# Kernel optimization log

Measured on AMD Instinct MI355X. Metric: run time of the kernel, lower is better.

Reference implementation:

```python
import jax, jax.numpy as jnp
import numpy as np

# Dims: batch, seq, model dim, heads, routes-per-query, bleed-over alpha
B, S, D, H, K_ROUTES = 4, 512, 1024, 16, 64
HD = D // H                      # head_dim = 64
SCALE = 1.0 / float(np.sqrt(HD))
ALPHA = 0.25                     # neighbor bleed-over (forward arg default 0.0; >0 here)
CAUSAL = True
NEG = jnp.float32(-1e9)


def _build_routes(seq_len: int, k: int, depth: int = 8) -> np.ndarray:
    """Cantor-coordinate based positional routes (mirrors _build_positional_routes)."""
    pos = np.arange(seq_len, dtype=np.float64)
    x = pos / max(1, seq_len - 1)
    x = np.clip(x, 1e-6, 1.0 - 1e-6)
    val = np.zeros_like(x)
    factor = 0.5
    for _ in range(depth):
        xs = x * 3.0
        digit = xs.astype(np.int64)
        frac = xs - digit
        val = val + (digit == 2).astype(np.float64) * factor
        x = frac
        factor *= 0.5
    coords = np.clip(val, 0.0, 1.0)
    dist = np.abs(coords[:, None] - coords[None, :])            # [S,S]
    routes = np.argsort(dist, axis=1, kind='stable')[:, :k]     # k smallest distances
    return routes.astype(np.int32)


def setup_inputs() -> dict:
    key = jax.random.key(0)
    k0, k1, k2 = jax.random.split(key, 3)
    x = jax.random.normal(k0, (B, S, D), dtype=jnp.float32)
    # nn.Linear weights stored pre-transposed as [in, out] for clean matmul
    w_qkv = jax.random.normal(k1, (D, 3 * D), dtype=jnp.float32) * (1.0 / np.sqrt(D))
    b_qkv = jnp.zeros((3 * D,), dtype=jnp.float32)
    w_out = jax.random.normal(k2, (D, D), dtype=jnp.float32) * (1.0 / np.sqrt(D))
    b_out = jnp.zeros((D,), dtype=jnp.float32)
    routes = jnp.asarray(_build_routes(S, K_ROUTES), dtype=jnp.int32)  # [S, K]
    return {"x": x, "w_qkv": w_qkv, "b_qkv": b_qkv,
            "w_out": w_out, "b_out": b_out, "routes": routes}


def reference(x, w_qkv, b_qkv, w_out, b_out, routes):
    # QKV projection: [B,S,3D] -> [3,B,H,S,hd]
    qkv = (x @ w_qkv + b_qkv).reshape(B, S, 3, H, HD).transpose(2, 0, 3, 1, 4)
    q, k, v = qkv[0], qkv[1], qkv[2]                 # each [B,H,S,hd]

    r = routes                                        # [S,K]
    k_g = jnp.take(k, r, axis=2)                      # [B,H,S,K,hd]
    v_g = jnp.take(v, r, axis=2)
    if ALPHA > 0.0:
        rl = jnp.clip(r - 1, 0, S - 1)
        rr = jnp.clip(r + 1, 0, S - 1)
        k_g = (1.0 - ALPHA) * k_g + (ALPHA / 2.0) * (jnp.take(k, rl, axis=2) + jnp.take(k, rr, axis=2))
        v_g = (1.0 - ALPHA) * v_g + (ALPHA / 2.0) * (jnp.take(v, rl, axis=2) + jnp.take(v, rr, axis=2))

    scores = jnp.einsum('bhqd,bhqkd->bhqk', q, k_g) * SCALE   # [B,H,S,K]
    if CAUSAL:
        # route index > query position is masked (each query always routes to itself)
        mask = r > jnp.arange(S, dtype=r.dtype)[:, None]       # [S,K]
        scores = jnp.where(mask[None, None], NEG, scores)

    attn = jax.nn.softmax(scores, axis=-1)
    out = jnp.einsum('bhqk,bhqkd->bhqd', attn, v_g)            # [B,H,S,hd]
    out = out.transpose(0, 2, 1, 3).reshape(B, S, D)
    return out @ w_out + b_out
```

## Files before the change

### kernel.cpp

```cpp
#include <hip/hip_runtime.h>
#include <hip/hip_bf16.h>

#define BB 4
#define SS 512
#define DD 1024
#define HH 16
#define KR 64
#define HDIM 64
#define THREE_D 3072
#define M_ROWS 2048
#define SCALE_F 0.125f

typedef __attribute__((ext_vector_type(8))) short short8;
typedef __attribute__((ext_vector_type(4))) float floatx4;

union F8 { short8 s; unsigned int u[4]; unsigned short h[8]; };

__device__ inline float bfu(unsigned short h){ union{unsigned int u; float f;} c; c.u = ((unsigned int)h) << 16; return c.f; }
__device__ inline unsigned short f2bf(float f){
    union{float f; unsigned int u;} c; c.f = f;
    unsigned int u = c.u;
    return (unsigned short)((u + 0x7fffu + ((u >> 16) & 1u)) >> 16);
}

#define GLOAD_LDS16(g, l)                                                     \
    __builtin_amdgcn_global_load_lds(                                         \
        (const __attribute__((address_space(1))) unsigned int*)(g),           \
        (__attribute__((address_space(3))) unsigned int*)(l), 16, 0, 0)

__global__ __launch_bounds__(256) void cvtA_kernel(const float* __restrict__ x,
                                                   unsigned short* __restrict__ out)
{
    int gid = blockIdx.x * 256 + threadIdx.x;
    int r  = gid & 127;
    int c  = (gid >> 7) & 3;
    int kt = (gid >> 9) & 31;
    int mt = gid >> 14;
    const float* src = x + ((size_t)(mt * 128 + r)) * 1024 + kt * 32 + c * 8;
    float4 a = *(const float4*)src;
    float4 b = *(const float4*)(src + 4);
    F8 o;
    o.h[0] = f2bf(a.x); o.h[1] = f2bf(a.y); o.h[2] = f2bf(a.z); o.h[3] = f2bf(a.w);
    o.h[4] = f2bf(b.x); o.h[5] = f2bf(b.y); o.h[6] = f2bf(b.z); o.h[7] = f2bf(b.w);
    *(uint4*)(out + (size_t)gid * 8) = *(uint4*)&o;
}

__global__ __launch_bounds__(256) void cvtB_kernel(const float* __restrict__ w,
                                                   unsigned short* __restrict__ out, int N)
{
    int gid = blockIdx.x * 256 + threadIdx.x;
    int r  = gid & 127;
    int c  = (gid >> 7) & 3;
    int kt = (gid >> 9) & 31;
    int nt = gid >> 14;
    int n = nt * 128 + r;
    int kbase = kt * 32 + c * 8;
    F8 o;
#pragma unroll
    for (int j = 0; j < 8; ++j)
        o.h[j] = f2bf(w[(size_t)(kbase + j) * N + n]);
    *(uint4*)(out + (size_t)gid * 8) = *(uint4*)&o;
}

__global__ __launch_bounds__(256) void gemm_qkv(
    const unsigned short* __restrict__ Asw,
    const unsigned short* __restrict__ Bsw,
    const float* __restrict__ bias,
    unsigned short* __restrict__ qb, unsigned short* __restrict__ kb,
    unsigned short* __restrict__ vb)
{
    __shared__ __align__(16) unsigned short Sh[128 * 136];
    unsigned short* Alds = Sh;
    unsigned short* Blds = Sh + 4096;

    const int tid  = threadIdx.x;
    const int lane = tid & 63;
    const int wid  = tid >> 6;
    const int l15  = lane & 15;
    const int quad = lane >> 4;
    const int wm   = (wid >> 1) * 64;
    const int wn   = (wid & 1) * 64;

    const unsigned short* Ak = Asw + (size_t)blockIdx.y * 131072;
    const unsigned short* Bk = Bsw + (size_t)blockIdx.x * 131072;

    floatx4 acc[4][4];
#pragma unroll
    for (int i = 0; i < 4; ++i)
#pragma unroll
        for (int j = 0; j < 4; ++j) acc[i][j] = (floatx4){0.f, 0.f, 0.f, 0.f};

    for (int kt = 0; kt < 32; ++kt) {
        const unsigned short* ga = Ak + kt * 4096 + wid * 1024 + lane * 8;
        const unsigned short* gb = Bk + kt * 4096 + wid * 1024 + lane * 8;
        GLOAD_LDS16(ga,       Alds + wid * 1024);
        GLOAD_LDS16(ga + 512, Alds + wid * 1024 + 512);
        GLOAD_LDS16(gb,       Blds + wid * 1024);
        GLOAD_LDS16(gb + 512, Blds + wid * 1024 + 512);
        __syncthreads();

        F8 af[4], bf[4];
#pragma unroll
        for (int mi = 0; mi < 4; ++mi)
            af[mi] = *(const F8*)(Alds + (size_t)(quad * 128 + wm + mi * 16 + l15) * 8);
#pragma unroll
        for (int ni = 0; ni < 4; ++ni)
            bf[ni] = *(const F8*)(Blds + (size_t)(quad * 128 + wn + ni * 16 + l15) * 8);
#pragma unroll
        for (int mi = 0; mi < 4; ++mi)
#pragma unroll
            for (int ni = 0; ni < 4; ++ni)
                acc[mi][ni] = __builtin_amdgcn_mfma_f32_16x16x32_bf16(
                    af[mi].s, bf[ni].s, acc[mi][ni], 0, 0, 0);
        __syncthreads();
    }

    const int m0 = blockIdx.y * 128;
    const int n0 = blockIdx.x * 128;

#pragma unroll
    for (int mi = 0; mi < 4; ++mi) {
#pragma unroll
        for (int ni = 0; ni < 4; ++ni) {
            int col = wn + ni * 16 + l15;
            float bv = bias[n0 + col];
#pragma unroll
            for (int r = 0; r < 4; ++r) {
                int row = wm + mi * 16 + quad * 4 + r;
                Sh[row * 136 + col] = f2bf(acc[mi][ni][r] + bv);
            }
        }
    }
    __syncthreads();

    for (int i = tid; i < 2048; i += 256) {
        int rr = i >> 4, cc = i & 15;
        int grow = m0 + rr, gcol = n0 + cc * 8;
        int b = grow >> 9, s = grow & 511;
        int which = gcol >> 10, rem = gcol & 1023;
        int h = rem >> 6, hd = rem & 63;
        unsigned short* dst = (which == 0) ? qb : (which == 1) ? kb : vb;
        uint4 val = *(const uint4*)(Sh + rr * 136 + cc * 8);
        *(uint4*)(dst + (((size_t)(b * HH + h) * SS) + s) * HDIM + hd) = val;
    }
}

__global__ __launch_bounds__(256) void gemm_out(
    const unsigned short* __restrict__ Asw,
    const unsigned short* __restrict__ Bsw,
    const float* __restrict__ bias,
    float* __restrict__ Cout)
{
    __shared__ __align__(16) unsigned short Alds[2048];
    __shared__ __align__(16) unsigned short Blds[4096];

    const int tid  = threadIdx.x;
    const int lane = tid & 63;
    const int wid  = tid >> 6;
    const int l15  = lane & 15;
    const int quad = lane >> 4;
    const int mt64 = blockIdx.y;
    const int mt   = mt64 >> 1;
    const int rh   = (mt64 & 1) * 64;
    const int nt   = blockIdx.x;
    const int wn   = wid * 32;

    floatx4 acc[4][2];
#pragma unroll
    for (int i = 0; i < 4; ++i)
#pragma unroll
        for (int j = 0; j < 2; ++j) acc[i][j] = (floatx4){0.f, 0.f, 0.f, 0.f};

    for (int kt = 0; kt < 32; ++kt) {
        const unsigned short* ga = Asw + ((size_t)(mt * 32 + kt) * 4 + wid) * 1024 + (rh + lane) * 8;
        const unsigned short* gb = Bsw + (size_t)(nt * 32 + kt) * 4096 + wid * 1024 + lane * 8;
        GLOAD_LDS16(ga,       Alds + (wid * 64 + lane) * 8);
        GLOAD_LDS16(gb,       Blds + wid * 1024 + lane * 8);
        GLOAD_LDS16(gb + 512, Blds + wid * 1024 + 512 + lane * 8);
        __syncthreads();

        F8 af[4], bf[2];
#pragma unroll
        for (int mi = 0; mi < 4; ++mi)
            af[mi] = *(const F8*)(Alds + (size_t)(quad * 64 + mi * 16 + l15) * 8);
#pragma unroll
        for (int ni = 0; ni < 2; ++ni)
            bf[ni] = *(const F8*)(Blds + (size_t)(quad * 128 + wn + ni * 16 + l15) * 8);
#pragma unroll
        for (int mi = 0; mi < 4; ++mi)
#pragma unroll
            for (int ni = 0; ni < 2; ++ni)
                acc[mi][ni] = __builtin_amdgcn_mfma_f32_16x16x32_bf16(
                    af[mi].s, bf[ni].s, acc[mi][ni], 0, 0, 0);
        __syncthreads();
    }

    const int m0 = mt64 * 64;
    const int n0 = nt * 128;
#pragma unroll
    for (int mi = 0; mi < 4; ++mi) {
#pragma unroll
        for (int ni = 0; ni < 2; ++ni) {
            int col = n0 + wn + ni * 16 + l15;
            float bv = bias[col];
#pragma unroll
            for (int r = 0; r < 4; ++r) {
                int row = m0 + mi * 16 + quad * 4 + r;
                Cout[(size_t)row * DD + col] = acc[mi][ni][r] + bv;
            }
        }
    }
}

__global__ __launch_bounds__(256) void blend_tr_kernel(
    const unsigned short* __restrict__ kb, const unsigned short* __restrict__ vb,
    unsigned short* __restrict__ K2g, unsigned short* __restrict__ Vtg)
{
    __shared__ float kt[130][65];
    __shared__ float vt[130][65];
    const int bh = blockIdx.x >> 2;
    const int sb = (blockIdx.x & 3) * 128;
    const int tid = threadIdx.x;
    const unsigned short* kbase = kb + (size_t)bh * SS * HDIM;
    const unsigned short* vbase = vb + (size_t)bh * SS * HDIM;

    for (int i = tid; i < 130 * 8; i += 256) {
        int row = i >> 3, c8 = (i & 7) << 3;
        int s = sb + row - 1; s = s < 0 ? 0 : (s > SS - 1 ? SS - 1 : s);
        F8 kk = *(const F8*)(kbase + (size_t)s * 64 + c8);
        F8 vv = *(const F8*)(vbase + (size_t)s * 64 + c8);
#pragma unroll
        for (int j = 0; j < 8; ++j) {
            kt[row][c8 + j] = bfu(kk.h[j]);
            vt[row][c8 + j] = bfu(vv.h[j]);
        }
    }
    __syncthreads();

    for (int i = tid; i < 128 * 16; i += 256) {
        int sl = i >> 4, c4 = (i & 15) << 2;
        ushort4 o;
        o.x = f2bf(0.75f * kt[sl+1][c4+0] + 0.125f * (kt[sl][c4+0] + kt[sl+2][c4+0]));
        o.y = f2bf(0.75f * kt[sl+1][c4+1] + 0.125f * (kt[sl][c4+1] + kt[sl+2][c4+1]));
        o.z = f2bf(0.75f * kt[sl+1][c4+2] + 0.125f * (kt[sl][c4+2] + kt[sl+2][c4+2]));
        o.w = f2bf(0.75f * kt[sl+1][c4+3] + 0.125f * (kt[sl][c4+3] + kt[sl+2][c4+3]));
        *(ushort4*)(K2g + ((size_t)bh * SS + sb + sl) * 64 + c4) = o;
    }
    for (int i = tid; i < 64 * 32; i += 256) {
        int d = i >> 5, s4 = (i & 31) << 2;
        ushort4 o;
        o.x = f2bf(0.75f * vt[s4+1][d] + 0.125f * (vt[s4+0][d] + vt[s4+2][d]));
        o.y = f2bf(0.75f * vt[s4+2][d] + 0.125f * (vt[s4+1][d] + vt[s4+3][d]));
        o.z = f2bf(0.75f * vt[s4+3][d] + 0.125f * (vt[s4+2][d] + vt[s4+4][d]));
        o.w = f2bf(0.75f * vt[s4+4][d] + 0.125f * (vt[s4+3][d] + vt[s4+5][d]));
        *(ushort4*)(Vtg + ((size_t)bh * 64 + d) * SS + sb + s4) = o;
    }
}

__global__ __launch_bounds__(256) void mask_kernel(const int* __restrict__ routes,
                                                   unsigned int* __restrict__ maskg)
{
    int q = blockIdx.x * 256 + threadIdx.x;
    unsigned int w[16];
#pragma unroll
    for (int i = 0; i < 16; ++i) w[i] = 0u;
    for (int j = 0; j < KR; ++j) {
        int r = routes[q * KR + j];
        if (r <= q) w[r >> 5] |= 1u << (r & 31);
    }
#pragma unroll
    for (int sw = 0; sw < 16; ++sw) maskg[sw * SS + q] = w[sw];
}

__global__ __launch_bounds__(512, 2) void attn_kernel(
    const unsigned short* __restrict__ qb,
    const unsigned short* __restrict__ K2g,
    const unsigned short* __restrict__ Vtg,
    const unsigned int* __restrict__ maskg,
    unsigned short* __restrict__ attn_sw)
{
    __shared__ __align__(16) unsigned short Ks[512 * 64];
    __shared__ __align__(16) unsigned short Vs[64 * 512];
    __shared__ __align__(16) unsigned short Ps[8 * 16 * 64];

    const int bh = blockIdx.x >> 2;
    const int qt = blockIdx.x & 3;
    const int b = bh >> 4, h = bh & 15;
    const int tid  = threadIdx.x;
    const int lane = tid & 63;
    const int wid  = tid >> 6;
    const int l15  = lane & 15;
    const int quad = lane >> 4;

    {
        const uint4* src = (const uint4*)(K2g + (size_t)bh * (SS * 64));
        uint4* dst = (uint4*)Ks;
        for (int c = tid; c < 4096; c += 512) {
            int s = c >> 3, cc = c & 7;
            dst[(s << 3) | (cc ^ (s & 7))] = src[c];
        }
        const uint4* srcv = (const uint4*)(Vtg + (size_t)bh * (64 * SS));
        uint4* dstv = (uint4*)Vs;
        for (int c = tid; c < 4096; c += 512) {
            int d = c >> 6, sc = c & 63;
            dstv[(d << 6) | (sc & 56) | ((sc ^ d) & 7)] = srcv[c];
        }
    }
    __syncthreads();

    const int qbase = qt * 128 + wid * 16;
    const int q = qbase + l15;

    F8 qf[2];
    {
        const unsigned short* qrow = qb + ((size_t)bh * SS + q) * 64;
        qf[0] = *(const F8*)(qrow + quad * 8);
        qf[1] = *(const F8*)(qrow + 32 + quad * 8);
    }

    floatx4 accS[32];
#pragma unroll
    for (int st = 0; st < 32; ++st) {
        int srow = st * 16 + l15;
        const F8 k0 = *(const F8*)(Ks + (((srow << 3) | ( quad      ^ (srow & 7))) << 3));
        const F8 k1 = *(const F8*)(Ks + (((srow << 3) | ((4 + quad) ^ (srow & 7))) << 3));
        floatx4 a = (floatx4){0.f, 0.f, 0.f, 0.f};
        a = __builtin_amdgcn_mfma_f32_16x16x32_bf16(k0.s, qf[0].s, a, 0, 0, 0);
        a = __builtin_amdgcn_mfma_f32_16x16x32_bf16(k1.s, qf[1].s, a, 0, 0, 0);
        accS[st] = a;
    }

    float m = -1e30f;
    unsigned int mw = 0;
#pragma unroll
    for (int st = 0; st < 32; ++st) {
        if ((st & 1) == 0) mw = maskg[(st >> 1) * SS + q];
        int sbase = (st & 1) * 16 + quad * 4;
        floatx4 a = accS[st];
#pragma unroll
        for (int r = 0; r < 4; ++r) {
            float v = ((mw >> (sbase + r)) & 1u) ? a[r] * SCALE_F : -1e30f;
            a[r] = v;
            m = fmaxf(m, v);
        }
        accS[st] = a;
    }
    m = fmaxf(m, __shfl_xor(m, 16));
    m = fmaxf(m, __shfl_xor(m, 32));

    floatx4 accO[4];
#pragma unroll
    for (int dt = 0; dt < 4; ++dt) accO[dt] = (floatx4){0.f, 0.f, 0.f, 0.f};
    float lsum = 0.f;
    unsigned int* Pw = (unsigned int*)Ps + wid * 512;

#pragma unroll
    for (int ch = 0; ch < 8; ++ch) {
#pragma unroll
        for (int t = 0; t < 4; ++t) {
            floatx4 a = accS[ch * 4 + t];
            float e0 = __expf(a[0] - m), e1 = __expf(a[1] - m);
            float e2 = __expf(a[2] - m), e3 = __expf(a[3] - m);
            lsum += (e0 + e1) + (e2 + e3);
            unsigned int w0 = (unsigned int)f2bf(e0) | ((unsigned int)f2bf(e1) << 16);
            unsigned int w1 = (unsigned int)f2bf(e2) | ((unsigned int)f2bf(e3) << 16);
            int off0 = t * 8 + quad * 2;
            int off1 = off0 + 1;
            Pw[l15 * 32 + ((((off0 >> 2) ^ (l15 & 7)) << 2) | (off0 & 3))] = w0;
            Pw[l15 * 32 + ((((off1 >> 2) ^ (l15 & 7)) << 2) | (off1 & 3))] = w1;
        }
        F8 pa[2];
#pragma unroll
        for (int ks = 0; ks < 2; ++ks) {
            int ci = ks * 4 + quad;
            pa[ks] = *(const F8*)((const unsigned short*)(Pw + l15 * 32) +
                                  ((ci ^ (l15 & 7)) << 3));
        }
#pragma unroll
        for (int dt = 0; dt < 4; ++dt) {
            int d = dt * 16 + l15;
#pragma unroll
            for (int ks = 0; ks < 2; ++ks) {
                int sc = ch * 8 + ks * 4 + quad;
                const F8 bv = *(const F8*)(Vs + (((d << 6) | (sc & 56) | ((sc ^ d) & 7)) << 3));
                accO[dt] = __builtin_amdgcn_mfma_f32_16x16x32_bf16(pa[ks].s, bv.s, accO[dt], 0, 0, 0);
            }
        }
    }

    lsum += __shfl_xor(lsum, 16);
    lsum += __shfl_xor(lsum, 32);
    float inv = 1.0f / lsum;

    unsigned short* Ow = Ps + wid * 1024;
#pragma unroll
    for (int r = 0; r < 4; ++r) {
        float invr = __shfl(inv, quad * 4 + r);
#pragma unroll
        for (int dt = 0; dt < 4; ++dt)
            Ow[(quad * 4 + r) * 64 + dt * 16 + l15] = f2bf(accO[dt][r] * invr);
    }
#pragma unroll
    for (int i = 0; i < 2; ++i) {
        int ch = i * 64 + lane;
        int qlocal = ch >> 3, j = ch & 7;
        int qq = qt * 128 + wid * 16 + qlocal;
        int mrow = b * SS + qq;
        int mt = mrow >> 7, rr = mrow & 127;
        int kt2 = h * 2 + (j >> 2), c = j & 3;
        size_t gid = (((size_t)(mt * 32 + kt2) * 4 + c) * 128 + rr);
        *(uint4*)(attn_sw + gid * 8) = *(const uint4*)(Ow + qlocal * 64 + j * 8);
    }
}

extern "C" void kernel_launch(void* const* d_in, const int* in_sizes, int n_in,
                              void* d_out, int out_size, void* d_ws, size_t ws_size,
                              hipStream_t stream)
{
    const float* x     = (const float*)d_in[0];
    const float* w_qkv = (const float*)d_in[1];
    const float* b_qkv = (const float*)d_in[2];
    const float* w_out = (const float*)d_in[3];
    const float* b_out = (const float*)d_in[4];
    const int* routes  = (const int*)d_in[5];

    char* w = (char*)d_ws;
    unsigned short* xb_sw  = (unsigned short*)(w);
    unsigned short* wb1_sw = (unsigned short*)(w + (4u  << 20));
    unsigned short* wb2_sw = (unsigned short*)(w + (10u << 20));
    unsigned short* qbuf   = (unsigned short*)(w + (12u << 20));
    unsigned short* kbuf   = (unsigned short*)(w + (16u << 20));
    unsigned short* vbuf   = (unsigned short*)(w + (20u << 20));
    unsigned short* K2g    = (unsigned short*)(w + (24u << 20));
    unsigned short* Vtg    = (unsigned short*)(w + (28u << 20));
    unsigned short* attnsw = (unsigned short*)(w + (32u << 20));
    unsigned int*   maskg  = (unsigned int*)(w + (36u << 20));

    cvtA_kernel<<<1024, 256, 0, stream>>>(x, xb_sw);
    cvtB_kernel<<<1536, 256, 0, stream>>>(w_qkv, wb1_sw, THREE_D);
    cvtB_kernel<<<512, 256, 0, stream>>>(w_out, wb2_sw, DD);
    mask_kernel<<<2, 256, 0, stream>>>(routes, maskg);

    gemm_qkv<<<dim3(THREE_D / 128, M_ROWS / 128), 256, 0, stream>>>(
        xb_sw, wb1_sw, b_qkv, qbuf, kbuf, vbuf);

    blend_tr_kernel<<<256, 256, 0, stream>>>(kbuf, vbuf, K2g, Vtg);

    attn_kernel<<<256, 512, 0, stream>>>(qbuf, K2g, Vtg, maskg, attnsw);

    gemm_out<<<dim3(DD / 128, M_ROWS / 64), 256, 0, stream>>>(
        attnsw, wb2_sw, b_out, (float*)d_out);
}
```

Measured before the change: 163.4 us.

## Fuse prep kernels, move K blend into attention, double K-step per GEMM sync

Merges the three conversion kernels and the mask kernel into one prep launch to cut launch overhead. The K neighbor blend moves out of the separate blend kernel into the attention kernel's LDS fill, so the K2g intermediate is no longer written and read back. Both GEMMs now stage two K tiles per barrier pair, halving the number of syncs at the cost of larger LDS use. The attention kernel now does three global reads per K chunk plus the blend arithmetic, which adds load latency to its prologue.

```diff
diff --git a/kernel.cpp b/kernel.cpp
--- a/kernel.cpp
+++ b/kernel.cpp
@@ -28,38 +28,56 @@
         (const __attribute__((address_space(1))) unsigned int*)(g),           \
         (__attribute__((address_space(3))) unsigned int*)(l), 16, 0, 0)
 
-__global__ __launch_bounds__(256) void cvtA_kernel(const float* __restrict__ x,
-                                                   unsigned short* __restrict__ out)
-{
-    int gid = blockIdx.x * 256 + threadIdx.x;
-    int r  = gid & 127;
-    int c  = (gid >> 7) & 3;
-    int kt = (gid >> 9) & 31;
-    int mt = gid >> 14;
-    const float* src = x + ((size_t)(mt * 128 + r)) * 1024 + kt * 32 + c * 8;
-    float4 a = *(const float4*)src;
-    float4 b = *(const float4*)(src + 4);
-    F8 o;
-    o.h[0] = f2bf(a.x); o.h[1] = f2bf(a.y); o.h[2] = f2bf(a.z); o.h[3] = f2bf(a.w);
-    o.h[4] = f2bf(b.x); o.h[5] = f2bf(b.y); o.h[6] = f2bf(b.z); o.h[7] = f2bf(b.w);
-    *(uint4*)(out + (size_t)gid * 8) = *(uint4*)&o;
-}
-
-__global__ __launch_bounds__(256) void cvtB_kernel(const float* __restrict__ w,
-                                                   unsigned short* __restrict__ out, int N)
-{
-    int gid = blockIdx.x * 256 + threadIdx.x;
-    int r  = gid & 127;
-    int c  = (gid >> 7) & 3;
-    int kt = (gid >> 9) & 31;
-    int nt = gid >> 14;
-    int n = nt * 128 + r;
-    int kbase = kt * 32 + c * 8;
-    F8 o;
-#pragma unroll
-    for (int j = 0; j < 8; ++j)
-        o.h[j] = f2bf(w[(size_t)(kbase + j) * N + n]);
-    *(uint4*)(out + (size_t)gid * 8) = *(uint4*)&o;
+__global__ __launch_bounds__(256) void prep_kernel(
+    const float* __restrict__ x, const float* __restrict__ w_qkv,
+    const float* __restrict__ w_out, const int* __restrict__ routes,
+    unsigned short* __restrict__ xb_sw, unsigned short* __restrict__ wb1_sw,
+    unsigned short* __restrict__ wb2_sw, unsigned int* __restrict__ maskg)
+{
+    const int bx = blockIdx.x;
+    const int tid = threadIdx.x;
+    if (bx < 1024) {
+        int gid = bx * 256 + tid;
+        int r  = gid & 127;
+        int c  = (gid >> 7) & 3;
+        int kt = (gid >> 9) & 31;
+        int mt = gid >> 14;
+        const float* src = x + ((size_t)(mt * 128 + r)) * 1024 + kt * 32 + c * 8;
+        float4 a = *(const float4*)src;
+        float4 b = *(const float4*)(src + 4);
+        F8 o;
+        o.h[0] = f2bf(a.x); o.h[1] = f2bf(a.y); o.h[2] = f2bf(a.z); o.h[3] = f2bf(a.w);
+        o.h[4] = f2bf(b.x); o.h[5] = f2bf(b.y); o.h[6] = f2bf(b.z); o.h[7] = f2bf(b.w);
+        *(uint4*)(xb_sw + (size_t)gid * 8) = *(uint4*)&o;
+    } else if (bx < 3072) {
+        const float* w;
+        unsigned short* out;
+        int gid, N;
+        if (bx < 2560) { w = w_qkv; out = wb1_sw; N = THREE_D; gid = (bx - 1024) * 256 + tid; }
+        else           { w = w_out; out = wb2_sw; N = DD;      gid = (bx - 2560) * 256 + tid; }
+        int r  = gid & 127;
+        int c  = (gid >> 7) & 3;
+        int kt = (gid >> 9) & 31;
+        int nt = gid >> 14;
+        int n = nt * 128 + r;
+        int kbase = kt * 32 + c * 8;
+        F8 o;
+#pragma unroll
+        for (int j = 0; j < 8; ++j)
+            o.h[j] = f2bf(w[(size_t)(kbase + j) * N + n]);
+        *(uint4*)(out + (size_t)gid * 8) = *(uint4*)&o;
+    } else {
+        int q = (bx - 3072) * 256 + tid;
+        unsigned int w[16];
+#pragma unroll
+        for (int i = 0; i < 16; ++i) w[i] = 0u;
+        for (int j = 0; j < KR; ++j) {
+            int r = routes[q * KR + j];
+            if (r <= q) w[r >> 5] |= 1u << (r & 31);
+        }
+#pragma unroll
+        for (int sw = 0; sw < 16; ++sw) maskg[sw * SS + q] = w[sw];
+    }
 }
 
 __global__ __launch_bounds__(256) void gemm_qkv(
@@ -69,9 +87,9 @@
     unsigned short* __restrict__ qb, unsigned short* __restrict__ kb,
     unsigned short* __restrict__ vb)
 {
-    __shared__ __align__(16) unsigned short Sh[128 * 136];
+    __shared__ __align__(16) unsigned short Sh[17408];
     unsigned short* Alds = Sh;
-    unsigned short* Blds = Sh + 4096;
+    unsigned short* Blds = Sh + 8192;
 
     const int tid  = threadIdx.x;
     const int lane = tid & 63;
@@ -90,28 +108,34 @@
 #pragma unroll
         for (int j = 0; j < 4; ++j) acc[i][j] = (floatx4){0.f, 0.f, 0.f, 0.f};
 
-    for (int kt = 0; kt < 32; ++kt) {
-        const unsigned short* ga = Ak + kt * 4096 + wid * 1024 + lane * 8;
-        const unsigned short* gb = Bk + kt * 4096 + wid * 1024 + lane * 8;
-        GLOAD_LDS16(ga,       Alds + wid * 1024);
-        GLOAD_LDS16(ga + 512, Alds + wid * 1024 + 512);
-        GLOAD_LDS16(gb,       Blds + wid * 1024);
-        GLOAD_LDS16(gb + 512, Blds + wid * 1024 + 512);
+    for (int kt2 = 0; kt2 < 16; ++kt2) {
+#pragma unroll
+        for (int kh = 0; kh < 2; ++kh) {
+            const unsigned short* ga = Ak + (kt2 * 2 + kh) * 4096 + wid * 1024 + lane * 8;
+            const unsigned short* gb = Bk + (kt2 * 2 + kh) * 4096 + wid * 1024 + lane * 8;
+            GLOAD_LDS16(ga,       Alds + kh * 4096 + wid * 1024 + lane * 8);
+            GLOAD_LDS16(ga + 512, Alds + kh * 4096 + wid * 1024 + 512 + lane * 8);
+            GLOAD_LDS16(gb,       Blds + kh * 4096 + wid * 1024 + lane * 8);
+            GLOAD_LDS16(gb + 512, Blds + kh * 4096 + wid * 1024 + 512 + lane * 8);
+        }
         __syncthreads();
 
-        F8 af[4], bf[4];
-#pragma unroll
-        for (int mi = 0; mi < 4; ++mi)
-            af[mi] = *(const F8*)(Alds + (size_t)(quad * 128 + wm + mi * 16 + l15) * 8);
-#pragma unroll
-        for (int ni = 0; ni < 4; ++ni)
-            bf[ni] = *(const F8*)(Blds + (size_t)(quad * 128 + wn + ni * 16 + l15) * 8);
-#pragma unroll
-        for (int mi = 0; mi < 4; ++mi)
+#pragma unroll
+        for (int kh = 0; kh < 2; ++kh) {
+            F8 af[4], bf[4];
+#pragma unroll
+            for (int mi = 0; mi < 4; ++mi)
+                af[mi] = *(const F8*)(Alds + kh * 4096 + (size_t)(quad * 128 + wm + mi * 16 + l15) * 8);
 #pragma unroll
             for (int ni = 0; ni < 4; ++ni)
-                acc[mi][ni] = __builtin_amdgcn_mfma_f32_16x16x32_bf16(
-                    af[mi].s, bf[ni].s, acc[mi][ni], 0, 0, 0);
+                bf[ni] = *(const F8*)(Blds + kh * 4096 + (size_t)(quad * 128 + wn + ni * 16 + l15) * 8);
+#pragma unroll
+            for (int mi = 0; mi < 4; ++mi)
+#pragma unroll
+                for (int ni = 0; ni < 4; ++ni)
+                    acc[mi][ni] = __builtin_amdgcn_mfma_f32_16x16x32_bf16(
+                        af[mi].s, bf[ni].s, acc[mi][ni], 0, 0, 0);
+        }
         __syncthreads();
     }
 
@@ -151,8 +175,8 @@
     const float* __restrict__ bias,
     float* __restrict__ Cout)
 {
-    __shared__ __align__(16) unsigned short Alds[2048];
-    __shared__ __align__(16) unsigned short Blds[4096];
+    __shared__ __align__(16) unsigned short Alds[4096];
+    __shared__ __align__(16) unsigned short Blds[8192];
 
     const int tid  = threadIdx.x;
     const int lane = tid & 63;
@@ -171,27 +195,34 @@
 #pragma unroll
         for (int j = 0; j < 2; ++j) acc[i][j] = (floatx4){0.f, 0.f, 0.f, 0.f};
 
-    for (int kt = 0; kt < 32; ++kt) {
-        const unsigned short* ga = Asw + ((size_t)(mt * 32 + kt) * 4 + wid) * 1024 + (rh + lane) * 8;
-        const unsigned short* gb = Bsw + (size_t)(nt * 32 + kt) * 4096 + wid * 1024 + lane * 8;
-        GLOAD_LDS16(ga,       Alds + (wid * 64 + lane) * 8);
-        GLOAD_LDS16(gb,       Blds + wid * 1024 + lane * 8);
-        GLOAD_LDS16(gb + 512, Blds + wid * 1024 + 512 + lane * 8);
+    for (int kt2 = 0; kt2 < 16; ++kt2) {
+#pragma unroll
+        for (int kh = 0; kh < 2; ++kh) {
+            int kt = kt2 * 2 + kh;
+            const unsigned short* ga = Asw + ((size_t)(mt * 32 + kt) * 4 + wid) * 1024 + (rh + lane) * 8;
+            const unsigned short* gb = Bsw + (size_t)(nt * 32 + kt) * 4096 + wid * 1024 + lane * 8;
+            GLOAD_LDS16(ga,       Alds + kh * 2048 + wid * 512 + lane * 8);
+            GLOAD_LDS16(gb,       Blds + kh * 4096 + wid * 1024 + lane * 8);
+            GLOAD_LDS16(gb + 512, Blds + kh * 4096 + wid * 1024 + 512 + lane * 8);
+        }
         __syncthreads();
 
-        F8 af[4], bf[2];
-#pragma unroll
-        for (int mi = 0; mi < 4; ++mi)
-            af[mi] = *(const F8*)(Alds + (size_t)(quad * 64 + mi * 16 + l15) * 8);
-#pragma unroll
-        for (int ni = 0; ni < 2; ++ni)
-            bf[ni] = *(const F8*)(Blds + (size_t)(quad * 128 + wn + ni * 16 + l15) * 8);
-#pragma unroll
-        for (int mi = 0; mi < 4; ++mi)
+#pragma unroll
+        for (int kh = 0; kh < 2; ++kh) {
+            F8 af[4], bf[2];
+#pragma unroll
+            for (int mi = 0; mi < 4; ++mi)
+                af[mi] = *(const F8*)(Alds + kh * 2048 + (size_t)(quad * 64 + mi * 16 + l15) * 8);
 #pragma unroll
             for (int ni = 0; ni < 2; ++ni)
-                acc[mi][ni] = __builtin_amdgcn_mfma_f32_16x16x32_bf16(
-                    af[mi].s, bf[ni].s, acc[mi][ni], 0, 0, 0);
+                bf[ni] = *(const F8*)(Blds + kh * 4096 + (size_t)(quad * 128 + wn + ni * 16 + l15) * 8);
+#pragma unroll
+            for (int mi = 0; mi < 4; ++mi)
+#pragma unroll
+                for (int ni = 0; ni < 2; ++ni)
+                    acc[mi][ni] = __builtin_amdgcn_mfma_f32_16x16x32_bf16(
+                        af[mi].s, bf[ni].s, acc[mi][ni], 0, 0, 0);
+        }
         __syncthreads();
     }
 
@@ -212,40 +243,24 @@
     }
 }
 
-__global__ __launch_bounds__(256) void blend_tr_kernel(
-    const unsigned short* __restrict__ kb, const unsigned short* __restrict__ vb,
-    unsigned short* __restrict__ K2g, unsigned short* __restrict__ Vtg)
-{
-    __shared__ float kt[130][65];
+__global__ __launch_bounds__(256) void blend_v_kernel(
+    const unsigned short* __restrict__ vb, unsigned short* __restrict__ Vtg)
+{
     __shared__ float vt[130][65];
     const int bh = blockIdx.x >> 2;
     const int sb = (blockIdx.x & 3) * 128;
     const int tid = threadIdx.x;
-    const unsigned short* kbase = kb + (size_t)bh * SS * HDIM;
     const unsigned short* vbase = vb + (size_t)bh * SS * HDIM;
 
     for (int i = tid; i < 130 * 8; i += 256) {
         int row = i >> 3, c8 = (i & 7) << 3;
         int s = sb + row - 1; s = s < 0 ? 0 : (s > SS - 1 ? SS - 1 : s);
-        F8 kk = *(const F8*)(kbase + (size_t)s * 64 + c8);
         F8 vv = *(const F8*)(vbase + (size_t)s * 64 + c8);
 #pragma unroll
-        for (int j = 0; j < 8; ++j) {
-            kt[row][c8 + j] = bfu(kk.h[j]);
-            vt[row][c8 + j] = bfu(vv.h[j]);
-        }
+        for (int j = 0; j < 8; ++j) vt[row][c8 + j] = bfu(vv.h[j]);
     }
     __syncthreads();
 
-    for (int i = tid; i < 128 * 16; i += 256) {
-        int sl = i >> 4, c4 = (i & 15) << 2;
-        ushort4 o;
-        o.x = f2bf(0.75f * kt[sl+1][c4+0] + 0.125f * (kt[sl][c4+0] + kt[sl+2][c4+0]));
-        o.y = f2bf(0.75f * kt[sl+1][c4+1] + 0.125f * (kt[sl][c4+1] + kt[sl+2][c4+1]));
-        o.z = f2bf(0.75f * kt[sl+1][c4+2] + 0.125f * (kt[sl][c4+2] + kt[sl+2][c4+2]));
-        o.w = f2bf(0.75f * kt[sl+1][c4+3] + 0.125f * (kt[sl][c4+3] + kt[sl+2][c4+3]));
-        *(ushort4*)(K2g + ((size_t)bh * SS + sb + sl) * 64 + c4) = o;
-    }
     for (int i = tid; i < 64 * 32; i += 256) {
         int d = i >> 5, s4 = (i & 31) << 2;
         ushort4 o;
@@ -257,24 +272,9 @@
     }
 }
 
-__global__ __launch_bounds__(256) void mask_kernel(const int* __restrict__ routes,
-                                                   unsigned int* __restrict__ maskg)
-{
-    int q = blockIdx.x * 256 + threadIdx.x;
-    unsigned int w[16];
-#pragma unroll
-    for (int i = 0; i < 16; ++i) w[i] = 0u;
-    for (int j = 0; j < KR; ++j) {
-        int r = routes[q * KR + j];
-        if (r <= q) w[r >> 5] |= 1u << (r & 31);
-    }
-#pragma unroll
-    for (int sw = 0; sw < 16; ++sw) maskg[sw * SS + q] = w[sw];
-}
-
 __global__ __launch_bounds__(512, 2) void attn_kernel(
     const unsigned short* __restrict__ qb,
-    const unsigned short* __restrict__ K2g,
+    const unsigned short* __restrict__ kbuf,
     const unsigned short* __restrict__ Vtg,
     const unsigned int* __restrict__ maskg,
     unsigned short* __restrict__ attn_sw)
@@ -293,11 +293,20 @@
     const int quad = lane >> 4;
 
     {
-        const uint4* src = (const uint4*)(K2g + (size_t)bh * (SS * 64));
+        const unsigned short* kbh = kbuf + (size_t)bh * (SS * 64);
         uint4* dst = (uint4*)Ks;
         for (int c = tid; c < 4096; c += 512) {
             int s = c >> 3, cc = c & 7;
-            dst[(s << 3) | (cc ^ (s & 7))] = src[c];
+            int sm = s ? s - 1 : 0;
+            int sp = (s < SS - 1) ? s + 1 : SS - 1;
+            F8 k0 = *(const F8*)(kbh + (size_t)s  * 64 + cc * 8);
+            F8 km = *(const F8*)(kbh + (size_t)sm * 64 + cc * 8);
+            F8 kp = *(const F8*)(kbh + (size_t)sp * 64 + cc * 8);
+            F8 o;
+#pragma unroll
+            for (int j = 0; j < 8; ++j)
+                o.h[j] = f2bf(0.75f * bfu(k0.h[j]) + 0.125f * (bfu(km.h[j]) + bfu(kp.h[j])));
+            dst[(s << 3) | (cc ^ (s & 7))] = *(uint4*)&o;
         }
         const uint4* srcv = (const uint4*)(Vtg + (size_t)bh * (64 * SS));
         uint4* dstv = (uint4*)Vs;
@@ -431,22 +440,19 @@
     unsigned short* qbuf   = (unsigned short*)(w + (12u << 20));
     unsigned short* kbuf   = (unsigned short*)(w + (16u << 20));
     unsigned short* vbuf   = (unsigned short*)(w + (20u << 20));
-    unsigned short* K2g    = (unsigned short*)(w + (24u << 20));
-    unsigned short* Vtg    = (unsigned short*)(w + (28u << 20));
-    unsigned short* attnsw = (unsigned short*)(w + (32u << 20));
-    unsigned int*   maskg  = (unsigned int*)(w + (36u << 20));
-
-    cvtA_kernel<<<1024, 256, 0, stream>>>(x, xb_sw);
-    cvtB_kernel<<<1536, 256, 0, stream>>>(w_qkv, wb1_sw, THREE_D);
-    cvtB_kernel<<<512, 256, 0, stream>>>(w_out, wb2_sw, DD);
-    mask_kernel<<<2, 256, 0, stream>>>(routes, maskg);
+    unsigned short* Vtg    = (unsigned short*)(w + (24u << 20));
+    unsigned short* attnsw = (unsigned short*)(w + (28u << 20));
+    unsigned int*   maskg  = (unsigned int*)(w + (32u << 20));
+
+    prep_kernel<<<3074, 256, 0, stream>>>(x, w_qkv, w_out, routes,
+                                          xb_sw, wb1_sw, wb2_sw, maskg);
 
     gemm_qkv<<<dim3(THREE_D / 128, M_ROWS / 128), 256, 0, stream>>>(
         xb_sw, wb1_sw, b_qkv, qbuf, kbuf, vbuf);
 
-    blend_tr_kernel<<<256, 256, 0, stream>>>(kbuf, vbuf, K2g, Vtg);
-
-    attn_kernel<<<256, 512, 0, stream>>>(qbuf, K2g, Vtg, maskg, attnsw);
+    blend_v_kernel<<<256, 256, 0, stream>>>(vbuf, Vtg);
+
+    attn_kernel<<<256, 512, 0, stream>>>(qbuf, kbuf, Vtg, maskg, attnsw);
 
     gemm_out<<<dim3(DD / 128, M_ROWS / 64), 256, 0, stream>>>(
         attnsw, wb2_sw, b_out, (float*)d_out);
```

Result: faster. 151.4 us (-7.4%).
